# Optimization experiments

Hardware: AMD Instinct MI355X
Metric: run time of the kernel (lower is better)

Reference implementation:

```python
import jax, jax.numpy as jnp
import numpy as np

B, S, D = 2, 2048, 1024
H, HD = 16, 64
FF = 4096
LOCAL_W, RAND_P = 256, 0.2
EPS = 1e-5
NEG = -9e15


def _linear_params(key, din, dout):
    kw, kb = jax.random.split(key)
    bound = 1.0 / np.sqrt(din)
    W = jax.random.uniform(kw, (din, dout), jnp.float32, -bound, bound)
    b = jax.random.uniform(kb, (dout,), jnp.float32, -bound, bound)
    return W, b


def setup_inputs() -> dict:
    key = jax.random.key(0)
    ks = jax.random.split(key, 10)
    x = jax.random.normal(ks[0], (B, S, D), jnp.float32)
    # local + random mask, as in create_local_mask
    i = np.arange(S)[:, None]
    j = np.arange(S)[None, :]
    local = (np.abs(i - j) <= LOCAL_W // 2)
    rnd = np.asarray(jax.random.bernoulli(ks[1], RAND_P, (S, S)))
    mask = jnp.asarray(np.logical_or(local, rnd).astype(np.int32))
    Wq, bq = _linear_params(ks[2], D, D)
    Wk, bk = _linear_params(ks[3], D, D)
    Wv, bv = _linear_params(ks[4], D, D)
    Wo, bo = _linear_params(ks[5], D, D)
    W1, b1 = _linear_params(ks[6], D, FF)
    W2, b2 = _linear_params(ks[7], FF, D)
    g1 = jnp.ones((D,), jnp.float32); be1 = jnp.zeros((D,), jnp.float32)
    g2 = jnp.ones((D,), jnp.float32); be2 = jnp.zeros((D,), jnp.float32)
    return dict(x=x, mask=mask, Wq=Wq, bq=bq, Wk=Wk, bk=bk, Wv=Wv, bv=bv,
                Wo=Wo, bo=bo, W1=W1, b1=b1, W2=W2, b2=b2,
                g1=g1, be1=be1, g2=g2, be2=be2)


def _layernorm(x, g, b):
    mu = jnp.mean(x, axis=-1, keepdims=True)
    var = jnp.mean(jnp.square(x - mu), axis=-1, keepdims=True)
    return (x - mu) * jax.lax.rsqrt(var + EPS) * g + b


def reference(x, mask, Wq, bq, Wk, bk, Wv, bv, Wo, bo, W1, b1, W2, b2, g1, be1, g2, be2):
    scale = jnp.float32(np.sqrt(HD))  # sqrt(head_dim), requires_grad=False
    q = x @ Wq + bq
    k = x @ Wk + bk
    v = x @ Wv + bv
    # faithful to original: view(B, heads, S, head_dim) WITHOUT transpose
    q = q.reshape(B, H, S, HD)
    k = k.reshape(B, H, S, HD)
    v = v.reshape(B, H, S, HD)
    scores = jnp.einsum('bhsd,bhtd->bhst', q / scale, k)  # [B,H,S,S]
    scores = jnp.where(mask == 0, jnp.float32(NEG), scores)
    probs = jax.nn.softmax(scores, axis=-1)
    av = jnp.einsum('bhst,bhtd->bhsd', probs, v)
    # faithful reshape back: view(B, S, head_dim*heads)
    attn_out = av.reshape(B, S, H * HD) @ Wo + bo
    x = _layernorm(x + attn_out, g1, be1)
    ffn = jax.nn.gelu(x @ W1 + b1, approximate=False) @ W2 + b2
    x = _layernorm(x + ffn, g2, be2)
    return x
```

## Files before the change

### kernel.cpp

```cpp
#include <hip/hip_runtime.h>
#include <cstdint>
#include <cstddef>

namespace {

constexpr int kS  = 2048;
constexpr int kD  = 1024;
constexpr int kHD = 64;
constexpr int kTOK = 4096;

typedef float f32x4 __attribute__((ext_vector_type(4)));
typedef __bf16 bf16x8 __attribute__((ext_vector_type(8)));
typedef unsigned short u16x8 __attribute__((ext_vector_type(8)));

__device__ __forceinline__ unsigned short f2b(float f){
  unsigned int u = __builtin_bit_cast(unsigned int, f);
  u += 0x7fffu + ((u >> 16) & 1u);
  return (unsigned short)(u >> 16);
}

__device__ __forceinline__ float b2f(unsigned short u){
  return __builtin_bit_cast(float, (unsigned)u << 16);
}

__device__ __forceinline__ bf16x8 ldfrag(const unsigned short* p){
  return __builtin_bit_cast(bf16x8, *(const u16x8*)p);
}

__device__ __forceinline__ float fexp2(float x){
#if __has_builtin(__builtin_amdgcn_exp2f)
  return __builtin_amdgcn_exp2f(x);
#else
  return exp2f(x);
#endif
}

__device__ __forceinline__ float fast_erf(float x){
  const float ax = fabsf(x);
#if __has_builtin(__builtin_amdgcn_rcpf)
  const float t = __builtin_amdgcn_rcpf(1.0f + 0.3275911f * ax);
#else
  const float t = 1.0f / (1.0f + 0.3275911f * ax);
#endif
  const float y = t * (0.254829592f + t * (-0.284496736f + t * (1.421413741f +
                  t * (-1.453152027f + t * 1.061405429f))));
  const float e = fexp2(-ax * ax * 1.4426950408889634f);
  return copysignf(1.0f - y * e, x);
}

__device__ __forceinline__ void gl_lds16(const void* g, void* l){
  __builtin_amdgcn_global_load_lds(
      (__attribute__((address_space(1))) void*)(void*)g,
      (__attribute__((address_space(3))) void*)l, 16, 0, 0);
}

__device__ __forceinline__ bf16x8 ld_swz(const unsigned short* tile, int row, int slot){
  return ldfrag(tile + row * 64 + (((slot ^ row) & 7) << 3));
}

__device__ __forceinline__ void stageK8(const unsigned short* Kg, unsigned short* lds,
                                        int tid, int t0){
  const int r = tid >> 3, sl = tid & 7;
  const int sabs = t0 + r;
  gl_lds16(Kg + (size_t)(sabs >> 4) * 3072 + (sabs & 15) * 64 + (((sl ^ r) & 7) << 3),
           (char*)lds + tid * 16);
}

__device__ __forceinline__ void stageV8(const unsigned short* Vh, unsigned short* lds,
                                        int tid, int t0){
  const int r = tid >> 3, sl = tid & 7;
  gl_lds16(Vh + (size_t)r * kS + t0 + (((sl ^ r) & 7) << 3),
           (char*)lds + tid * 16);
}

__global__ __launch_bounds__(256) void prep_misc_kern(const float* __restrict__ x,
                                                      unsigned short* __restrict__ xb,
                                                      const int* __restrict__ mask,
                                                      unsigned long long* __restrict__ mb,
                                                      const float* __restrict__ bq,
                                                      const float* __restrict__ bk,
                                                      const float* __restrict__ bv,
                                                      float* __restrict__ bqkv){
  const int b = blockIdx.x;
  if (b < 4096){
    const int i = b * 256 + threadIdx.x;
    float4 v = ((const float4*)x)[i];
    ((ushort4*)xb)[i] = make_ushort4(f2b(v.x), f2b(v.y), f2b(v.z), f2b(v.w));
  } else if (b < 20480){
    const int gw   = ((b - 4096) * 256 + threadIdx.x) >> 6;
    const int lane = threadIdx.x & 63;
    const int row  = gw >> 5, word = gw & 31;
    const int key  = ((lane >> 2) & 3) * 16 + ((lane >> 4) & 3) * 4 + (lane & 3);
    const int m = mask[(size_t)row * kS + word * 64 + key];
    const unsigned long long bl = __ballot(m != 0);
    if (lane == 0) mb[(size_t)row * 32 + word] = bl;
  } else {
    const int i = (b - 20480) * 256 + threadIdx.x;
    float v = (i < 1024) ? bq[i] : ((i < 2048) ? bk[i - 1024] : bv[i - 2048]);
    bqkv[i] = v;
  }
}

__global__ __launch_bounds__(256) void wtrans_all_kern(const float* __restrict__ Wq,
                                                       const float* __restrict__ Wk,
                                                       const float* __restrict__ Wv,
                                                       const float* __restrict__ Wo,
                                                       const float* __restrict__ W1,
                                                       const float* __restrict__ W2,
                                                       unsigned short* __restrict__ WqkvT,
                                                       unsigned short* __restrict__ WoT,
                                                       unsigned short* __restrict__ W1T,
                                                       unsigned short* __restrict__ W2T){
  const int b = blockIdx.x;
  const float* W; unsigned short* Wt; int K, N, nx, lb;
  if      (b < 1024){ W = Wq; Wt = WqkvT;                 K = 1024; N = 1024; nx = 32;  lb = b; }
  else if (b < 2048){ W = Wk; Wt = WqkvT + 1024 * 1024;   K = 1024; N = 1024; nx = 32;  lb = b - 1024; }
  else if (b < 3072){ W = Wv; Wt = WqkvT + 2048 * 1024;   K = 1024; N = 1024; nx = 32;  lb = b - 2048; }
  else if (b < 4096){ W = Wo; Wt = WoT;                   K = 1024; N = 1024; nx = 32;  lb = b - 3072; }
  else if (b < 8192){ W = W1; Wt = W1T;                   K = 1024; N = 4096; nx = 128; lb = b - 4096; }
  else              { W = W2; Wt = W2T;                   K = 4096; N = 1024; nx = 32;  lb = b - 8192; }
  __shared__ float t[32][33];
  const int n0 = (lb % nx) * 32, k0 = (lb / nx) * 32;
  const int tx = threadIdx.x & 31, ty = threadIdx.x >> 5;
  #pragma unroll
  for (int i = 0; i < 32; i += 8)
    t[ty + i][tx] = W[(size_t)(k0 + ty + i) * N + n0 + tx];
  __syncthreads();
  #pragma unroll
  for (int i = 0; i < 32; i += 8)
    Wt[(size_t)(n0 + ty + i) * K + k0 + tx] = f2b(t[tx][ty + i]);
}

__global__ __launch_bounds__(256) void vtrans_kern(const unsigned short* __restrict__ QKV,
                                                   unsigned short* __restrict__ Vt){
  __shared__ unsigned short t[64][65];
  int bh = blockIdx.y, s0 = blockIdx.x * 64;
  const int rowbase = (bh >> 4) * 2048 + (bh & 15) * 128;
  const unsigned short* Vg = QKV + (size_t)rowbase * 3072 + 2048;
  unsigned short* Vth = Vt + (size_t)bh * kHD * kS;
  int tx = threadIdx.x & 63, ty = threadIdx.x >> 6;
  #pragma unroll
  for (int i = 0; i < 64; i += 4){
    const int s = s0 + ty + i;
    t[ty + i][tx] = Vg[(size_t)(s >> 4) * 3072 + (s & 15) * 64 + tx];
  }
  __syncthreads();
  #pragma unroll
  for (int i = 0; i < 64; i += 4)
    Vth[(size_t)(ty + i) * kS + s0 + tx] = t[tx][ty + i];
}

template <int ACT_GELU, int SPLITK, int SCLQ>
__global__ __launch_bounds__(512, 2) void gemm256_kern(const unsigned short* __restrict__ A,
                                                       const unsigned short* __restrict__ Bt,
                                                       const float* __restrict__ bias,
                                                       unsigned short* __restrict__ C,
                                                       int M, int N, int K){
  __shared__ unsigned short As[2][2][128 * 64];
  __shared__ unsigned short Bs[2][2][128 * 64];
  int bid = blockIdx.y * gridDim.x + blockIdx.x;
  const int nwg = gridDim.x * gridDim.y;
  bid = (bid & 7) * (nwg >> 3) + (bid >> 3);
  const int bx = bid % gridDim.x, by = bid / gridDim.x;
  const int m0 = by << 8, n0 = bx << 8;
  const int tid  = threadIdx.x;
  const int wave = tid >> 6, lane = tid & 63;
  const int wr = wave >> 2, wc = wave & 3;
  const int lr = lane & 15, lk = lane >> 4;
  const int kz   = K / SPLITK;
  const int kbeg = (SPLITK > 1) ? blockIdx.z * kz : 0;
  const int NT   = kz >> 6;
  const int srow = tid >> 3;
  const int scol = ((tid & 7) ^ (srow & 7)) << 3;
  const unsigned short* Ag = A  + (size_t)(m0 + srow) * K + kbeg + scol;
  const unsigned short* Bg = Bt + (size_t)(n0 + srow) * K + kbeg + scol;
  const int dst = tid * 8;
  const int sk0 = ((    lk) ^ (lr & 7)) << 3;
  const int sk1 = ((4 + lk) ^ (lr & 7)) << 3;
  const int aro = lr * 64;
  const int bro = ((wc & 1) * 64 + lr) * 64;
  const int bh_ = wc >> 1;

  f32x4 acc[8][4] = {};
  bf16x8 aR[4][2], bR[2][2][2];

  auto stA = [&](int b, int h, int kt){
    const unsigned short* s = Ag + (size_t)(h * 128) * K + kt * 64;
    gl_lds16(s,                  &As[b][h][dst]);
    gl_lds16(s + (size_t)64 * K, &As[b][h][4096 + dst]);
  };
  auto stB = [&](int b, int h, int kt){
    const unsigned short* s = Bg + (size_t)(h * 128) * K + kt * 64;
    gl_lds16(s,                  &Bs[b][h][dst]);
    gl_lds16(s + (size_t)64 * K, &Bs[b][h][4096 + dst]);
  };

#define LOAD_A(b, MH) { \
  _Pragma("unroll") for (int mp = 0; mp < 4; ++mp){ \
    aR[mp][0] = ldfrag(&As[b][wr][aro + ((MH) * 64 + mp * 16) * 64 + sk0]); \
    aR[mp][1] = ldfrag(&As[b][wr][aro + ((MH) * 64 + mp * 16) * 64 + sk1]); } }
#define LOAD_B(b, NH) { \
  _Pragma("unroll") for (int np = 0; np < 2; ++np){ \
    bR[NH][np][0] = ldfrag(&Bs[b][bh_][bro + ((NH) * 32 + np * 16) * 64 + sk0]); \
    bR[NH][np][1] = ldfrag(&Bs[b][bh_][bro + ((NH) * 32 + np * 16) * 64 + sk1]); } }
#define QMFMA(MH, NH) { \
  _Pragma("unroll") for (int kk = 0; kk < 2; ++kk) \
  _Pragma("unroll") for (int mp = 0; mp < 4; ++mp) \
  _Pragma("unroll") for (int np = 0; np < 2; ++np) \
    acc[(MH)*4+mp][(NH)*2+np] = __builtin_amdgcn_mfma_f32_16x16x32_bf16( \
        aR[mp][kk], bR[NH][np][kk], acc[(MH)*4+mp][(NH)*2+np], 0, 0, 0); }

  stA(0, 0, 0); stB(0, 0, 0);
  stA(0, 1, 0); stB(0, 1, 0);
  asm volatile("s_waitcnt vmcnt(4)" ::: "memory");

  for (int t = 0; t < NT; ++t){
    const int b = t & 1, bn = b ^ 1;
    const bool pf = (t + 1 < NT);
    if (pf){ stA(bn, 0, t + 1); stB(bn, 0, t + 1);
             asm volatile("s_waitcnt vmcnt(4)" ::: "memory"); }
    else   { asm volatile("s_waitcnt vmcnt(0)" ::: "memory"); }
    asm volatile("s_barrier" ::: "memory");
    LOAD_A(b, 0);
    LOAD_B(b, 0);
    LOAD_B(b, 1);
    __builtin_amdgcn_s_setprio(1);
    QMFMA(0, 0);
    QMFMA(0, 1);
    __builtin_amdgcn_s_setprio(0);
    if (pf){ stA(bn, 1, t + 1); stB(bn, 1, t + 1);
             asm volatile("s_waitcnt vmcnt(4)" ::: "memory"); }
    asm volatile("s_barrier" ::: "memory");
    LOAD_A(b, 1);
    __builtin_amdgcn_s_setprio(1);
    QMFMA(1, 0);
    QMFMA(1, 1);
    __builtin_amdgcn_s_setprio(0);
  }
#undef LOAD_A
#undef LOAD_B
#undef QMFMA

  unsigned short* Cb = C + (SPLITK > 1 ? (size_t)blockIdx.z * M * N : 0);
  float bvv[4], csc[4];
  #pragma unroll
  for (int n = 0; n < 4; ++n){
    const int col = n0 + wc * 64 + n * 16 + lr;
    bvv[n] = (SPLITK == 1) ? bias[col] : 0.0f;
    csc[n] = (SCLQ && col < 1024) ? 0.18033688011112042f : 1.0f;
  }
  #pragma unroll
  for (int m = 0; m < 8; ++m){
    #pragma unroll
    for (int j = 0; j < 4; ++j){
      const int row = m0 + wr * 128 + m * 16 + lk * 4 + j;
      unsigned short* crow = Cb + (size_t)row * N + n0 + wc * 64 + lr;
      #pragma unroll
      for (int n = 0; n < 4; ++n){
        float v = acc[m][n][j] + bvv[n];
        if (ACT_GELU) v = 0.5f * v * (1.0f + fast_erf(v * 0.70710678118654752f));
        if (SCLQ) v *= csc[n];
        crow[n * 16] = f2b(v);
      }
    }
  }
}

__global__ __launch_bounds__(512) void attn_kern(const unsigned short* __restrict__ QKV,
                                                 const unsigned short* __restrict__ Vt,
                                                 const unsigned long long* __restrict__ mbits,
                                                 unsigned short* __restrict__ O){
  __shared__ unsigned short Ks[3][64 * 64];
  __shared__ unsigned short Vs[3][64 * 64];
  __shared__ unsigned short Ps[8][16 * 64];
  const int tid = threadIdx.x;
  const int wave = tid >> 6, lane = tid & 63;
  const int lr = lane & 15, lk = lane >> 4;
  int bid = blockIdx.y * gridDim.x + blockIdx.x;
  bid = (bid & 7) * 64 + (bid >> 3);
  const int qblk = bid & 15, bh = bid >> 4;
  const int rowbase = (bh >> 4) * 2048 + (bh & 15) * 128;
  const unsigned short* Qg = QKV + (size_t)rowbase * 3072;
  const unsigned short* Kg = Qg + 1024;
  const unsigned short* Vh = Vt + (size_t)bh * kHD * kS;
  const int qbase = qblk * 128 + wave * 16;
  constexpr int NT = kS / 64;

  bf16x8 qf[2];
  { const int qr = qbase + lr;
    const unsigned short* qp = Qg + (size_t)(qr >> 4) * 3072 + (qr & 15) * 64 + lk * 8;
    qf[0] = ldfrag(qp); qf[1] = ldfrag(qp + 32); }

  f32x4 accO[4] = {};
  float lsum = 0.f;
  unsigned short* Pw = Ps[wave];
  char* Pwb = (char*)Pw + lr * 128 + ((lk & 1) << 3);
  const int lr7 = lr & 7;

  const unsigned long long* mrp = mbits + (size_t)(qbase + lr) * 32;
  unsigned long long mb = mrp[0];

  stageK8(Kg, Ks[0], tid, 0);
  stageV8(Vh, Vs[0], tid, 0);
  stageK8(Kg, Ks[1], tid, 64);
  stageV8(Vh, Vs[1], tid, 64);
  asm volatile("s_waitcnt vmcnt(2)" ::: "memory");
  asm volatile("s_barrier" ::: "memory");

  int cur = 0, stg = 2;
  for (int t = 0; t < NT; ++t){
    unsigned long long mbn = 0;
    if (t < NT - 1) mbn = mrp[t + 1];
    if (t < NT - 2){
      stageK8(Kg, Ks[stg], tid, (t + 2) * 64);
      stageV8(Vh, Vs[stg], tid, (t + 2) * 64);
    }
    f32x4 sa[4] = {};
    #pragma unroll
    for (int kk = 0; kk < 2; ++kk)
      #pragma unroll
      for (int n = 0; n < 4; ++n){
        bf16x8 kf = ld_swz(Ks[cur], n * 16 + lr, kk * 4 + lk);
        sa[n] = __builtin_amdgcn_mfma_f32_16x16x32_bf16(kf, qf[kk], sa[n], 0, 0, 0);
      }
    const unsigned wb = (unsigned)(mb >> (lk * 16));
    float s = 0.f;
    #pragma unroll
    for (int n = 0; n < 4; ++n){
      float p0, p1, p2, p3;
      {
        float v0 = fexp2(sa[n][0]), v1 = fexp2(sa[n][1]);
        float v2 = fexp2(sa[n][2]), v3 = fexp2(sa[n][3]);
        const int s0 = ((int)(wb << (31 - (n * 4 + 0)))) >> 31;
        const int s1 = ((int)(wb << (31 - (n * 4 + 1)))) >> 31;
        const int s2 = ((int)(wb << (31 - (n * 4 + 2)))) >> 31;
        const int s3 = ((int)(wb << (31 - (n * 4 + 3)))) >> 31;
        p0 = __builtin_bit_cast(float, __builtin_bit_cast(int, v0) & s0);
        p1 = __builtin_bit_cast(float, __builtin_bit_cast(int, v1) & s1);
        p2 = __builtin_bit_cast(float, __builtin_bit_cast(int, v2) & s2);
        p3 = __builtin_bit_cast(float, __builtin_bit_cast(int, v3) & s3);
      }
      s += (p0 + p1) + (p2 + p3);
      unsigned r0, r1;
      asm("v_cvt_pk_bf16_f32 %0, %1, %2" : "=v"(r0) : "v"(p0), "v"(p1));
      asm("v_cvt_pk_bf16_f32 %0, %1, %2" : "=v"(r1) : "v"(p2), "v"(p3));
      *(uint2*)(Pwb + (((2 * n + (lk >> 1)) ^ lr7) << 4)) = make_uint2(r0, r1);
    }
    s += __shfl_xor(s, 16);
    s += __shfl_xor(s, 32);
    lsum += s;
    #pragma unroll
    for (int kk = 0; kk < 2; ++kk){
      bf16x8 pf = ld_swz(Pw, lr, kk * 4 + lk);
      #pragma unroll
      for (int dd = 0; dd < 4; ++dd){
        bf16x8 vfr = ld_swz(Vs[cur], dd * 16 + lr, kk * 4 + lk);
        accO[dd] = __builtin_amdgcn_mfma_f32_16x16x32_bf16(pf, vfr, accO[dd], 0, 0, 0);
      }
    }
    mb = mbn;
    if (t < NT - 2){
      asm volatile("s_waitcnt vmcnt(3)" ::: "memory");
    } else if (t < NT - 1){
      asm volatile("s_waitcnt vmcnt(1)" ::: "memory");
    }
    if (t < NT - 1) asm volatile("s_barrier" ::: "memory");
    cur = (cur == 2) ? 0 : cur + 1;
    stg = (stg == 2) ? 0 : stg + 1;
  }
  const size_t hoff = (size_t)bh * kS * kHD;
  #pragma unroll
  for (int j = 0; j < 4; ++j){
    const float inv = 1.0f / __shfl(lsum, lk * 4 + j);
    const int row = qbase + lk * 4 + j;
    #pragma unroll
    for (int dd = 0; dd < 4; ++dd)
      O[hoff + (size_t)row * 64 + dd * 16 + lr] = f2b(accO[dd][j] * inv);
  }
}

template <int NP, int PBF16, int OUT_B>
__global__ __launch_bounds__(256) void add_ln_kern(const float* __restrict__ X,
                                                   const void* __restrict__ P,
                                                   const float* __restrict__ bias,
                                                   const float* __restrict__ g,
                                                   const float* __restrict__ be,
                                                   float* __restrict__ Yf,
                                                   unsigned short* __restrict__ Yb){
  const int row = blockIdx.x;
  const int tid = threadIdx.x;
  const size_t pstride = (size_t)kTOK * kD;
  const int idx = row * 256 + tid;
  float r0 = 0.f, r1 = 0.f, r2 = 0.f, r3 = 0.f;
  #pragma unroll
  for (int z = 0; z < NP; ++z){
    if (PBF16){
      ushort4 u = ((const ushort4*)P)[z * (pstride / 4) + idx];
      r0 += b2f(u.x); r1 += b2f(u.y); r2 += b2f(u.z); r3 += b2f(u.w);
    } else {
      float4 p = ((const float4*)P)[z * (pstride / 4) + idx];
      r0 += p.x; r1 += p.y; r2 += p.z; r3 += p.w;
    }
  }
  const float4 bb = ((const float4*)bias)[tid];
  const float4 xv = ((const float4*)X)[idx];
  const float a0 = xv.x + r0 + bb.x, a1 = xv.y + r1 + bb.y;
  const float a2 = xv.z + r2 + bb.z, a3 = xv.w + r3 + bb.w;
  float s = a0 + a1 + a2 + a3;
  float q = a0*a0 + a1*a1 + a2*a2 + a3*a3;
  #pragma unroll
  for (int d = 1; d < 64; d <<= 1){ s += __shfl_xor(s, d); q += __shfl_xor(q, d); }
  __shared__ float red[8];
  const int wave = tid >> 6, lane = tid & 63;
  if (lane == 0){ red[wave] = s; red[4 + wave] = q; }
  __syncthreads();
  s = red[0] + red[1] + red[2] + red[3];
  q = red[4] + red[5] + red[6] + red[7];
  const float mu   = s * (1.0f / kD);
  const float var  = q * (1.0f / kD) - mu * mu;
  const float rstd = rsqrtf(var + 1e-5f);
  const float4 gv = ((const float4*)g)[tid];
  const float4 bv = ((const float4*)be)[tid];
  const float y0 = (a0 - mu) * rstd * gv.x + bv.x;
  const float y1 = (a1 - mu) * rstd * gv.y + bv.y;
  const float y2 = (a2 - mu) * rstd * gv.z + bv.z;
  const float y3 = (a3 - mu) * rstd * gv.w + bv.w;
  ((float4*)Yf)[idx] = make_float4(y0, y1, y2, y3);
  if (OUT_B)
    ((ushort4*)Yb)[idx] = make_ushort4(f2b(y0), f2b(y1), f2b(y2), f2b(y3));
}

}

extern "C" void kernel_launch(void* const* d_in, const int* in_sizes, int n_in,
                              void* d_out, int out_size, void* d_ws, size_t ws_size,
                              hipStream_t stream){
  (void)in_sizes; (void)n_in; (void)out_size;
  const float* x   = (const float*)d_in[0];
  const int*   mask= (const int*)d_in[1];
  const float* Wq  = (const float*)d_in[2];  const float* bq  = (const float*)d_in[3];
  const float* Wk  = (const float*)d_in[4];  const float* bk  = (const float*)d_in[5];
  const float* Wv  = (const float*)d_in[6];  const float* bv  = (const float*)d_in[7];
  const float* Wo  = (const float*)d_in[8];  const float* bo  = (const float*)d_in[9];
  const float* W1  = (const float*)d_in[10]; const float* b1  = (const float*)d_in[11];
  const float* W2  = (const float*)d_in[12]; const float* b2  = (const float*)d_in[13];
  const float* g1  = (const float*)d_in[14]; const float* be1 = (const float*)d_in[15];
  const float* g2  = (const float*)d_in[16]; const float* be2 = (const float*)d_in[17];

  char* ws = (char*)d_ws;
  const size_t MB = 1024 * 1024;
  if (ws_size < 96 * MB) return;

  unsigned short* W2T   = (unsigned short*)(ws + 0 * MB);
  unsigned short* W1T   = (unsigned short*)(ws + 8 * MB);
  unsigned short* WqkvT = (unsigned short*)(ws + 16 * MB);
  unsigned short* WoT   = (unsigned short*)(ws + 22 * MB);
  unsigned short* xb    = (unsigned short*)(ws + 24 * MB);
  unsigned short* qkv   = (unsigned short*)(ws + 32 * MB);
  unsigned short* vt    = (unsigned short*)(ws + 56 * MB);
  unsigned short* av    = (unsigned short*)(ws + 64 * MB);
  unsigned long long* mbits = (unsigned long long*)(ws + 72 * MB);
  float* bqkv           = (float*)(ws + 80 * MB);
  unsigned short* woP   = (unsigned short*)(ws + 32 * MB);
  float* y32            = (float*)(ws + 72 * MB);
  unsigned short* yb    = (unsigned short*)(ws + 88 * MB);
  unsigned short* hb    = (unsigned short*)(ws + 40 * MB);
  unsigned short* w2p   = (unsigned short*)(ws + 8 * MB);

  dim3 blk(256), gblk(512);
  wtrans_all_kern<<<dim3(12288), blk, 0, stream>>>(Wq, Wk, Wv, Wo, W1, W2,
                                                   WqkvT, WoT, W1T, W2T);
  prep_misc_kern<<<dim3(20492), blk, 0, stream>>>(x, xb, mask, mbits, bq, bk, bv, bqkv);

  gemm256_kern<0,1,1><<<dim3(12, 16), gblk, 0, stream>>>(xb, WqkvT, bqkv, qkv, 4096, 3072, 1024);

  vtrans_kern<<<dim3(32, 32), blk, 0, stream>>>(qkv, vt);
  attn_kern<<<dim3(16, 32), gblk, 0, stream>>>(qkv, vt, mbits, av);

  gemm256_kern<0,4,0><<<dim3(4, 16, 4), gblk, 0, stream>>>(av, WoT, bo, woP, 4096, 1024, 1024);
  add_ln_kern<4,1,1><<<dim3(4096), blk, 0, stream>>>(x, woP, bo, g1, be1, y32, yb);

  gemm256_kern<1,1,0><<<dim3(16, 16), gblk, 0, stream>>>(yb, W1T, b1, hb, 4096, 4096, 1024);
  gemm256_kern<0,4,0><<<dim3(4, 16, 4), gblk, 0, stream>>>(hb, W2T, b2, w2p, 4096, 1024, 4096);
  add_ln_kern<4,1,0><<<dim3(4096), blk, 0, stream>>>(y32, w2p, b2, g2, be2, (float*)d_out, nullptr);
}
```

Before: 230.2 us.

## Replace 256x256 GEMM tiles with 128x128 tiles using 256-thread blocks

The GEMM kernel moves from 256x256 output tiles with 8 waves and a split-phase double-buffered pipeline to 128x128 tiles with 4 waves, each computing a 64x64 sub-tile. Grids grow fourfold, so the 304 CUs on MI355X get more blocks and fewer sit idle, especially on the QKV and FF1 GEMMs, which had only 192 and 256 blocks. The cost is lower arithmetic intensity per tile, meaning more global and LDS traffic per FLOP. The simpler single-phase loop also gives less overlap between loads and MFMA work.

```diff
diff --git a/kernel.cpp b/kernel.cpp
--- a/kernel.cpp
+++ b/kernel.cpp
@@ -151,21 +151,21 @@
 }
 
 template <int ACT_GELU, int SPLITK, int SCLQ>
-__global__ __launch_bounds__(512, 2) void gemm256_kern(const unsigned short* __restrict__ A,
+__global__ __launch_bounds__(256, 2) void gemm128_kern(const unsigned short* __restrict__ A,
                                                        const unsigned short* __restrict__ Bt,
                                                        const float* __restrict__ bias,
                                                        unsigned short* __restrict__ C,
                                                        int M, int N, int K){
-  __shared__ unsigned short As[2][2][128 * 64];
-  __shared__ unsigned short Bs[2][2][128 * 64];
+  __shared__ unsigned short As[2][128 * 64];
+  __shared__ unsigned short Bs[2][128 * 64];
   int bid = blockIdx.y * gridDim.x + blockIdx.x;
   const int nwg = gridDim.x * gridDim.y;
   bid = (bid & 7) * (nwg >> 3) + (bid >> 3);
   const int bx = bid % gridDim.x, by = bid / gridDim.x;
-  const int m0 = by << 8, n0 = bx << 8;
+  const int m0 = by << 7, n0 = bx << 7;
   const int tid  = threadIdx.x;
   const int wave = tid >> 6, lane = tid & 63;
-  const int wr = wave >> 2, wc = wave & 3;
+  const int wr = wave >> 1, wc = wave & 1;
   const int lr = lane & 15, lk = lane >> 4;
   const int kz   = K / SPLITK;
   const int kbeg = (SPLITK > 1) ? blockIdx.z * kz : 0;
@@ -177,69 +177,54 @@
   const int dst = tid * 8;
   const int sk0 = ((    lk) ^ (lr & 7)) << 3;
   const int sk1 = ((4 + lk) ^ (lr & 7)) << 3;
-  const int aro = lr * 64;
-  const int bro = ((wc & 1) * 64 + lr) * 64;
-  const int bh_ = wc >> 1;
-
-  f32x4 acc[8][4] = {};
-  bf16x8 aR[4][2], bR[2][2][2];
-
-  auto stA = [&](int b, int h, int kt){
-    const unsigned short* s = Ag + (size_t)(h * 128) * K + kt * 64;
-    gl_lds16(s,                  &As[b][h][dst]);
-    gl_lds16(s + (size_t)64 * K, &As[b][h][4096 + dst]);
+  const int aro = (wr * 64 + lr) * 64;
+  const int bro = (wc * 64 + lr) * 64;
+
+  f32x4 acc[4][4] = {};
+
+  auto stage = [&](int b, int kt){
+    const unsigned short* a = Ag + (size_t)kt * 64;
+    const unsigned short* g = Bg + (size_t)kt * 64;
+    #pragma unroll
+    for (int i = 0; i < 4; ++i)
+      gl_lds16(a + (size_t)(i * 32) * K, &As[b][i * 2048 + dst]);
+    #pragma unroll
+    for (int i = 0; i < 4; ++i)
+      gl_lds16(g + (size_t)(i * 32) * K, &Bs[b][i * 2048 + dst]);
   };
-  auto stB = [&](int b, int h, int kt){
-    const unsigned short* s = Bg + (size_t)(h * 128) * K + kt * 64;
-    gl_lds16(s,                  &Bs[b][h][dst]);
-    gl_lds16(s + (size_t)64 * K, &Bs[b][h][4096 + dst]);
-  };
-
-#define LOAD_A(b, MH) { \
-  _Pragma("unroll") for (int mp = 0; mp < 4; ++mp){ \
-    aR[mp][0] = ldfrag(&As[b][wr][aro + ((MH) * 64 + mp * 16) * 64 + sk0]); \
-    aR[mp][1] = ldfrag(&As[b][wr][aro + ((MH) * 64 + mp * 16) * 64 + sk1]); } }
-#define LOAD_B(b, NH) { \
-  _Pragma("unroll") for (int np = 0; np < 2; ++np){ \
-    bR[NH][np][0] = ldfrag(&Bs[b][bh_][bro + ((NH) * 32 + np * 16) * 64 + sk0]); \
-    bR[NH][np][1] = ldfrag(&Bs[b][bh_][bro + ((NH) * 32 + np * 16) * 64 + sk1]); } }
-#define QMFMA(MH, NH) { \
-  _Pragma("unroll") for (int kk = 0; kk < 2; ++kk) \
-  _Pragma("unroll") for (int mp = 0; mp < 4; ++mp) \
-  _Pragma("unroll") for (int np = 0; np < 2; ++np) \
-    acc[(MH)*4+mp][(NH)*2+np] = __builtin_amdgcn_mfma_f32_16x16x32_bf16( \
-        aR[mp][kk], bR[NH][np][kk], acc[(MH)*4+mp][(NH)*2+np], 0, 0, 0); }
-
-  stA(0, 0, 0); stB(0, 0, 0);
-  stA(0, 1, 0); stB(0, 1, 0);
-  asm volatile("s_waitcnt vmcnt(4)" ::: "memory");
+
+  stage(0, 0);
+  asm volatile("s_waitcnt vmcnt(0)" ::: "memory");
+  asm volatile("s_barrier" ::: "memory");
 
   for (int t = 0; t < NT; ++t){
-    const int b = t & 1, bn = b ^ 1;
+    const int b = t & 1;
     const bool pf = (t + 1 < NT);
-    if (pf){ stA(bn, 0, t + 1); stB(bn, 0, t + 1);
-             asm volatile("s_waitcnt vmcnt(4)" ::: "memory"); }
-    else   { asm volatile("s_waitcnt vmcnt(0)" ::: "memory"); }
-    asm volatile("s_barrier" ::: "memory");
-    LOAD_A(b, 0);
-    LOAD_B(b, 0);
-    LOAD_B(b, 1);
+    if (pf){ stage(b ^ 1, t + 1); asm volatile("s_waitcnt vmcnt(8)" ::: "memory"); }
+    else   {                      asm volatile("s_waitcnt vmcnt(0)" ::: "memory"); }
+    bf16x8 aR[4][2], bR[4][2];
+    #pragma unroll
+    for (int m = 0; m < 4; ++m){
+      aR[m][0] = ldfrag(&As[b][aro + m * 1024 + sk0]);
+      aR[m][1] = ldfrag(&As[b][aro + m * 1024 + sk1]);
+    }
+    #pragma unroll
+    for (int n = 0; n < 4; ++n){
+      bR[n][0] = ldfrag(&Bs[b][bro + n * 1024 + sk0]);
+      bR[n][1] = ldfrag(&Bs[b][bro + n * 1024 + sk1]);
+    }
     __builtin_amdgcn_s_setprio(1);
-    QMFMA(0, 0);
-    QMFMA(0, 1);
+    #pragma unroll
+    for (int kk = 0; kk < 2; ++kk)
+      #pragma unroll
+      for (int m = 0; m < 4; ++m)
+        #pragma unroll
+        for (int n = 0; n < 4; ++n)
+          acc[m][n] = __builtin_amdgcn_mfma_f32_16x16x32_bf16(
+              aR[m][kk], bR[n][kk], acc[m][n], 0, 0, 0);
     __builtin_amdgcn_s_setprio(0);
-    if (pf){ stA(bn, 1, t + 1); stB(bn, 1, t + 1);
-             asm volatile("s_waitcnt vmcnt(4)" ::: "memory"); }
-    asm volatile("s_barrier" ::: "memory");
-    LOAD_A(b, 1);
-    __builtin_amdgcn_s_setprio(1);
-    QMFMA(1, 0);
-    QMFMA(1, 1);
-    __builtin_amdgcn_s_setprio(0);
-  }
-#undef LOAD_A
-#undef LOAD_B
-#undef QMFMA
+    if (pf) asm volatile("s_barrier" ::: "memory");
+  }
 
   unsigned short* Cb = C + (SPLITK > 1 ? (size_t)blockIdx.z * M * N : 0);
   float bvv[4], csc[4];
@@ -250,10 +235,10 @@
     csc[n] = (SCLQ && col < 1024) ? 0.18033688011112042f : 1.0f;
   }
   #pragma unroll
-  for (int m = 0; m < 8; ++m){
+  for (int m = 0; m < 4; ++m){
     #pragma unroll
     for (int j = 0; j < 4; ++j){
-      const int row = m0 + wr * 128 + m * 16 + lk * 4 + j;
+      const int row = m0 + wr * 64 + m * 16 + lk * 4 + j;
       unsigned short* crow = Cb + (size_t)row * N + n0 + wc * 64 + lr;
       #pragma unroll
       for (int n = 0; n < 4; ++n){
@@ -472,15 +457,15 @@
                                                    WqkvT, WoT, W1T, W2T);
   prep_misc_kern<<<dim3(20492), blk, 0, stream>>>(x, xb, mask, mbits, bq, bk, bv, bqkv);
 
-  gemm256_kern<0,1,1><<<dim3(12, 16), gblk, 0, stream>>>(xb, WqkvT, bqkv, qkv, 4096, 3072, 1024);
+  gemm128_kern<0,1,1><<<dim3(24, 32), blk, 0, stream>>>(xb, WqkvT, bqkv, qkv, 4096, 3072, 1024);
 
   vtrans_kern<<<dim3(32, 32), blk, 0, stream>>>(qkv, vt);
   attn_kern<<<dim3(16, 32), gblk, 0, stream>>>(qkv, vt, mbits, av);
 
-  gemm256_kern<0,4,0><<<dim3(4, 16, 4), gblk, 0, stream>>>(av, WoT, bo, woP, 4096, 1024, 1024);
+  gemm128_kern<0,4,0><<<dim3(8, 32, 4), blk, 0, stream>>>(av, WoT, bo, woP, 4096, 1024, 1024);
   add_ln_kern<4,1,1><<<dim3(4096), blk, 0, stream>>>(x, woP, bo, g1, be1, y32, yb);
 
-  gemm256_kern<1,1,0><<<dim3(16, 16), gblk, 0, stream>>>(yb, W1T, b1, hb, 4096, 4096, 1024);
-  gemm256_kern<0,4,0><<<dim3(4, 16, 4), gblk, 0, stream>>>(hb, W2T, b2, w2p, 4096, 1024, 4096);
+  gemm128_kern<1,1,0><<<dim3(32, 32), blk, 0, stream>>>(yb, W1T, b1, hb, 4096, 4096, 1024);
+  gemm128_kern<0,4,0><<<dim3(8, 32, 4), blk, 0, stream>>>(hb, W2T, b2, w2p, 4096, 1024, 4096);
   add_ln_kern<4,1,0><<<dim3(4096), blk, 0, stream>>>(y32, w2p, b2, g2, be2, (float*)d_out, nullptr);
 }
```

New measurement: 258.1 us. +12.1%, slower.
